# Kernel tuning notes

Measured on AMD Instinct MI355X. Metric: run time of the kernel, lower is better.

The kernel has to match this reference:

```python
import math
import jax, jax.numpy as jnp
import numpy as np

D_IN, R_S, T_MAX = 1024, 256, 2048
B, T = 8, 2048


def setup_inputs() -> dict:
    key = jax.random.key(0)
    ks = jax.random.split(key, 8)
    u = jax.random.normal(ks[0], (B, T, D_IN), dtype=jnp.float32)
    h0_r = jax.random.normal(ks[1], (B, R_S), dtype=jnp.float32)
    h0_i = jax.random.normal(ks[2], (B, R_S), dtype=jnp.float32)
    # parameters (lambda_raw randomized instead of zeros so sigmoid is nontrivial)
    lambda_raw = jax.random.normal(ks[3], (R_S,), dtype=jnp.float32)
    # omega init exactly as in the torch module
    log_min, log_max = math.log(1.0 / T_MAX), math.log(math.pi)
    n = np.arange(1, R_S + 1, dtype=np.float32)
    weyl_freqs = n * math.pi / R_S
    log_freqs = np.exp(np.linspace(log_min, log_max, R_S, dtype=np.float32))
    omega = jnp.asarray(0.5 * weyl_freqs + 0.5 * log_freqs, dtype=jnp.float32)
    W_proj = jax.random.normal(ks[4], (R_S, D_IN), dtype=jnp.float32) / math.sqrt(D_IN)
    W_res = jax.random.normal(ks[5], (2 * R_S, D_IN), dtype=jnp.float32) / math.sqrt(D_IN)
    ln_gamma = jnp.ones((2 * R_S,), dtype=jnp.float32)
    ln_beta = jnp.zeros((2 * R_S,), dtype=jnp.float32)
    return {"u": u, "h0_r": h0_r, "h0_i": h0_i, "lambda_raw": lambda_raw,
            "omega": omega, "W_proj": W_proj, "W_res": W_res,
            "ln_gamma": ln_gamma, "ln_beta": ln_beta}


def _layernorm(x, gamma, beta, eps=1e-5):
    mu = jnp.mean(x, axis=-1, keepdims=True)
    var = jnp.mean(jnp.square(x - mu), axis=-1, keepdims=True)
    return (x - mu) * jax.lax.rsqrt(var + eps) * gamma + beta


def reference(u, h0_r, h0_i, lambda_raw, omega, W_proj, W_res, ln_gamma, ln_beta):
    Bb, Tt, _ = u.shape
    lam = -jax.nn.sigmoid(lambda_raw) * 5.0                      # [R]
    t = jnp.arange(Tt, dtype=jnp.float32)                        # [T]
    decay = jnp.exp(lam[:, None] * t[None, :])                   # [R,T]
    phase = omega[:, None] * t[None, :]                          # [R,T]
    f_r = decay * jnp.cos(phase)
    f_i = decay * jnp.sin(phase)
    u_proj = jnp.einsum('btd,rd->brt', u, W_proj)                # [B,R,T]
    n_fft = 2 * Tt
    U_f = jnp.fft.rfft(u_proj, n=n_fft, axis=-1)                 # [B,R,F]
    F_r = jnp.fft.rfft(f_r, n=n_fft, axis=-1)[None]              # [1,R,F]
    F_i = jnp.fft.rfft(f_i, n=n_fft, axis=-1)[None]
    h_r = jnp.fft.irfft(U_f * F_r, n=n_fft, axis=-1)[..., :Tt]   # [B,R,T]
    h_i = jnp.fft.irfft(U_f * F_i, n=n_fft, axis=-1)[..., :Tt]
    # ZIR correction from initial state
    t_zir = t + 1.0
    decay_z = jnp.exp(lam[:, None] * t_zir[None, :])             # [R,T]
    phase_z = omega[:, None] * t_zir[None, :]
    f_r_z = decay_z * jnp.cos(phase_z)
    f_i_z = decay_z * jnp.sin(phase_z)
    h0r = h0_r[:, :, None]                                       # [B,R,1]
    h0i = h0_i[:, :, None]
    h_r = h_r + h0r * f_r_z[None] - h0i * f_i_z[None]
    h_i = h_i + h0r * f_i_z[None] + h0i * f_r_z[None]
    h_r = jnp.swapaxes(h_r, 1, 2)                                # [B,T,R]
    h_i = jnp.swapaxes(h_i, 1, 2)
    ssm_out = jnp.concatenate([h_r, h_i], axis=-1)               # [B,T,2R]
    res = jnp.einsum('btd,ed->bte', u, W_res)                    # [B,T,2R]
    out = _layernorm(ssm_out + res, ln_gamma, ln_beta)
    final_r = jax.lax.stop_gradient(h_r[:, -1])
    final_i = jax.lax.stop_gradient(h_i[:, -1])
    return out, final_r, final_i
```

## Files before the change

### kernel.cpp

```cpp
#include <hip/hip_runtime.h>
#include <math.h>

#define T_LEN 2048
#define BB    8
#define RS    256
#define DIN   1024
#define NE    768
#define M_TOT (BB * T_LEN)
#define LCH   32
#define NCH   (T_LEN / LCH)
#define OUT_MAIN (M_TOT * 512)

typedef unsigned short ushort;
typedef unsigned int   uint;
typedef short  short8  __attribute__((ext_vector_type(8)));
typedef float  f32x4   __attribute__((ext_vector_type(4)));
typedef ushort ushort8 __attribute__((ext_vector_type(8)));

__device__ __forceinline__ ushort f2bf_rn(float x) {
    uint u = __float_as_uint(x);
    return (ushort)((u + 0x7FFFu + ((u >> 16) & 1u)) >> 16);
}
__device__ __forceinline__ float bf2f(ushort b) {
    return __uint_as_float(((uint)b) << 16);
}

__device__ __forceinline__ void gload16(const ushort* g, ushort* l) {
    __builtin_amdgcn_global_load_lds(
        (const __attribute__((address_space(1))) uint*)g,
        (__attribute__((address_space(3))) uint*)l, 16, 0, 0);
}

#define N8U  (M_TOT * DIN / 8)
#define N8WP (RS * DIN / 8)
#define N8WR (2 * RS * DIN / 8)
#define N8TOT (N8U + N8WP + N8WR)

__global__ __launch_bounds__(256) void split_kernel(
    const float* __restrict__ u, const float* __restrict__ wp,
    const float* __restrict__ wr, ushort* __restrict__ Uhi,
    ushort* __restrict__ Ulo, ushort* __restrict__ Whi, ushort* __restrict__ Wlo)
{
    const int i = blockIdx.x * 256 + threadIdx.x;
    if (i >= N8TOT) return;
    const float* src; ushort* hi; ushort* lo; int j;
    if (i < N8U)              { src = u;  hi = Uhi; lo = Ulo; j = i; }
    else if (i < N8U + N8WP)  { src = wp; hi = Whi; lo = Wlo; j = i - N8U; }
    else                      { src = wr; hi = Whi + (size_t)RS * DIN;
                                lo = Wlo + (size_t)RS * DIN; j = i - N8U - N8WP; }
    const float4 x0 = ((const float4*)src)[(size_t)j * 2 + 0];
    const float4 x1 = ((const float4*)src)[(size_t)j * 2 + 1];
    const float xs[8] = {x0.x, x0.y, x0.z, x0.w, x1.x, x1.y, x1.z, x1.w};
    ushort8 hv, lv;
#pragma unroll
    for (int k = 0; k < 8; ++k) {
        const ushort hb = f2bf_rn(xs[k]);
        hv[k] = hb;
        lv[k] = f2bf_rn(xs[k] - bf2f(hb));
    }
    ((ushort8*)hi)[j] = hv;
    ((ushort8*)lo)[j] = lv;
}

#define Bb 128
#define BK 32

__global__ __launch_bounds__(256) void gemm_mfma(
    const ushort* __restrict__ Uh, const ushort* __restrict__ Ul,
    const ushort* __restrict__ Wh, const ushort* __restrict__ Wl,
    float* __restrict__ C)
{
    __shared__ ushort Ah[Bb * BK], Al[Bb * BK], Bh[Bb * BK], Bl[Bb * BK];
    const int tid  = threadIdx.x;
    const int bn   = blockIdx.x;
    const int bm   = blockIdx.y;
    const int wid  = tid >> 6;
    const int lane = tid & 63;
    const int wr   = wid >> 1, wc = wid & 1;
    const int fr   = lane & 15;
    const int fq   = lane >> 4;

    const int srow = tid >> 2;
    const int skk  = (tid & 3) * 8;
    const ushort* gAh = Uh + (size_t)(bm * 128 + srow) * DIN + skk;
    const ushort* gAl = Ul + (size_t)(bm * 128 + srow) * DIN + skk;
    const ushort* gBh = Wh + (size_t)(bn * 128 + srow) * DIN + skk;
    const ushort* gBl = Wl + (size_t)(bn * 128 + srow) * DIN + skk;
    ushort* lAh0 = Ah + tid * 8; ushort* lAh1 = Ah + 64 * BK + tid * 8;
    ushort* lAl0 = Al + tid * 8; ushort* lAl1 = Al + 64 * BK + tid * 8;
    ushort* lBh0 = Bh + tid * 8; ushort* lBh1 = Bh + 64 * BK + tid * 8;
    ushort* lBl0 = Bl + tid * 8; ushort* lBl1 = Bl + 64 * BK + tid * 8;
    const size_t rstep = (size_t)64 * DIN;

    f32x4 acc[4][4];
#pragma unroll
    for (int m = 0; m < 4; ++m)
#pragma unroll
        for (int n = 0; n < 4; ++n) acc[m][n] = (f32x4){0.f, 0.f, 0.f, 0.f};

    for (int kk = 0; kk < DIN; kk += BK) {
        gload16(gAh + kk, lAh0); gload16(gAh + kk + rstep, lAh1);
        gload16(gAl + kk, lAl0); gload16(gAl + kk + rstep, lAl1);
        gload16(gBh + kk, lBh0); gload16(gBh + kk + rstep, lBh1);
        gload16(gBl + kk, lBl0); gload16(gBl + kk + rstep, lBl1);
        __syncthreads();

        short8 ah[4], al[4], bh[4], bl[4];
#pragma unroll
        for (int m = 0; m < 4; ++m) {
            const int row = wr * 64 + m * 16 + fr;
            ah[m] = *(const short8*)&Ah[row * BK + fq * 8];
            al[m] = *(const short8*)&Al[row * BK + fq * 8];
        }
#pragma unroll
        for (int n = 0; n < 4; ++n) {
            const int col = wc * 64 + n * 16 + fr;
            bh[n] = *(const short8*)&Bh[col * BK + fq * 8];
            bl[n] = *(const short8*)&Bl[col * BK + fq * 8];
        }
#pragma unroll
        for (int m = 0; m < 4; ++m)
#pragma unroll
            for (int n = 0; n < 4; ++n) {
                acc[m][n] = __builtin_amdgcn_mfma_f32_16x16x32_bf16(ah[m], bh[n], acc[m][n], 0, 0, 0);
                acc[m][n] = __builtin_amdgcn_mfma_f32_16x16x32_bf16(ah[m], bl[n], acc[m][n], 0, 0, 0);
                acc[m][n] = __builtin_amdgcn_mfma_f32_16x16x32_bf16(al[m], bh[n], acc[m][n], 0, 0, 0);
            }
        __syncthreads();
    }

    const int crow0 = bm * 128 + wr * 64;
    const int ccol0 = bn * 128 + wc * 64;
#pragma unroll
    for (int m = 0; m < 4; ++m) {
        const int row = crow0 + m * 16 + fq * 4;
#pragma unroll
        for (int n = 0; n < 4; ++n) {
            const int col = ccol0 + n * 16 + fr;
#pragma unroll
            for (int j = 0; j < 4; ++j)
                C[(size_t)(row + j) * NE + col] = acc[m][n][j];
        }
    }
}

__device__ inline void pole(const float* __restrict__ lraw, const float* __restrict__ om,
                            int r, float& zr, float& zi, float& lam, float& o)
{
    const float x   = lraw[r];
    const float sig = 1.f / (1.f + expf(-x));
    lam = -5.f * sig;
    o   = om[r];
    const float er = expf(lam);
    zr = er * cosf(o);
    zi = er * sinf(o);
}

__global__ __launch_bounds__(256) void carry_kernel(
    const float* __restrict__ C, const float* __restrict__ lraw,
    const float* __restrict__ om, float2* __restrict__ carry)
{
    const int c = blockIdx.x, b = blockIdx.y, r = threadIdx.x;
    const int m0 = b * T_LEN + c * LCH;
    float zr, zi, lam, o;
    pole(lraw, om, r, zr, zi, lam, o);
    const float* p = C + (size_t)m0 * NE + r;
    float hr = 0.f, hi = 0.f;
#pragma unroll 8
    for (int s = 0; s < LCH; ++s) {
        const float u  = p[(size_t)s * NE];
        const float nr = zr * hr - zi * hi + u;
        const float ni = zr * hi + zi * hr;
        hr = nr; hi = ni;
    }
    carry[(size_t)(b * NCH + c) * RS + r] = make_float2(hr, hi);
}

__global__ __launch_bounds__(256) void chunk_scan_kernel(
    const float2* __restrict__ carry, const float* __restrict__ h0r,
    const float* __restrict__ h0i, const float* __restrict__ lraw,
    const float* __restrict__ om, float2* __restrict__ S, float* __restrict__ out)
{
    const int b = blockIdx.x, r = threadIdx.x;
    __shared__ float2 cs[32 * RS];
    float zr, zi, lam, o;
    pole(lraw, om, r, zr, zi, lam, o);
    const float eL  = expf(lam * (float)LCH);
    const float zLr = eL * cosf(o * (float)LCH);
    const float zLi = eL * sinf(o * (float)LCH);
    float sr = h0r[b * RS + r];
    float si = h0i[b * RS + r];
    for (int half = 0; half < 2; ++half) {
        __syncthreads();
        const float4* src = (const float4*)(carry + ((size_t)b * NCH + half * 32) * RS);
        float4* dst = (float4*)cs;
        for (int i = r; i < 32 * RS / 2; i += 256) dst[i] = src[i];
        __syncthreads();
        for (int cc = 0; cc < 32; ++cc) {
            const int c = half * 32 + cc;
            S[((size_t)b * NCH + c) * RS + r] = make_float2(sr, si);
            const float2 k = cs[cc * RS + r];
            const float nr = zLr * sr - zLi * si + k.x;
            const float ni = zLr * si + zLi * sr + k.y;
            sr = nr; si = ni;
        }
    }
    out[OUT_MAIN + b * RS + r]           = sr;
    out[OUT_MAIN + BB * RS + b * RS + r] = si;
}

__global__ __launch_bounds__(256) void scan_ln_kernel(
    const float* __restrict__ C, const float2* __restrict__ S,
    const float* __restrict__ lraw, const float* __restrict__ om,
    const float* __restrict__ gamma, const float* __restrict__ beta,
    float* __restrict__ out)
{
    const int c = blockIdx.x, b = blockIdx.y, r = threadIdx.x;
    __shared__ float tile[8][NE];
    const int m0 = b * T_LEN + c * LCH;
    float zr, zi, lam, o;
    pole(lraw, om, r, zr, zi, lam, o);
    float2 st = S[(size_t)(b * NCH + c) * RS + r];
    const int wid = r >> 6, lane = r & 63;
    const float4 g0  = *(const float4*)&gamma[lane * 8];
    const float4 g1  = *(const float4*)&gamma[lane * 8 + 4];
    const float4 be0 = *(const float4*)&beta[lane * 8];
    const float4 be1 = *(const float4*)&beta[lane * 8 + 4];

    float4 rv[6];
    {
        const float4* src = (const float4*)(C + (size_t)m0 * NE);
#pragma unroll
        for (int k = 0; k < 6; ++k) rv[k] = src[r + 256 * k];
#pragma unroll
        for (int k = 0; k < 6; ++k) ((float4*)tile)[r + 256 * k] = rv[k];
    }

    for (int batch = 0; batch < 4; ++batch) {
        __syncthreads();
        if (batch < 3) {
            const float4* src = (const float4*)(C + (size_t)(m0 + (batch + 1) * 8) * NE);
#pragma unroll
            for (int k = 0; k < 6; ++k) rv[k] = src[r + 256 * k];
        }
#pragma unroll
        for (int s = 0; s < 8; ++s) {
            const float u  = tile[s][r];
            const float hr = zr * st.x - zi * st.y + u;
            const float hi = zr * st.y + zi * st.x;
            st.x = hr; st.y = hi;
            tile[s][256 + r] = hr + tile[s][256 + r];
            tile[s][512 + r] = hi + tile[s][512 + r];
        }
        __syncthreads();
#pragma unroll
        for (int rr = 0; rr < 2; ++rr) {
            const int s = wid * 2 + rr;
            const int m = m0 + batch * 8 + s;
            const float4 x0 = *(const float4*)&tile[s][256 + lane * 8];
            const float4 x1 = *(const float4*)&tile[s][256 + lane * 8 + 4];
            float s1 = (x0.x + x0.y) + (x0.z + x0.w) + (x1.x + x1.y) + (x1.z + x1.w);
            float s2 = (x0.x * x0.x + x0.y * x0.y) + (x0.z * x0.z + x0.w * x0.w)
                     + (x1.x * x1.x + x1.y * x1.y) + (x1.z * x1.z + x1.w * x1.w);
#pragma unroll
            for (int off = 1; off < 64; off <<= 1) {
                s1 += __shfl_xor(s1, off);
                s2 += __shfl_xor(s2, off);
            }
            const float mu   = s1 * (1.f / 512.f);
            const float var  = s2 * (1.f / 512.f) - mu * mu;
            const float rstd = rsqrtf(var + 1e-5f);
            float4 o0, o1;
            o0.x = (x0.x - mu) * rstd * g0.x + be0.x;
            o0.y = (x0.y - mu) * rstd * g0.y + be0.y;
            o0.z = (x0.z - mu) * rstd * g0.z + be0.z;
            o0.w = (x0.w - mu) * rstd * g0.w + be0.w;
            o1.x = (x1.x - mu) * rstd * g1.x + be1.x;
            o1.y = (x1.y - mu) * rstd * g1.y + be1.y;
            o1.z = (x1.z - mu) * rstd * g1.z + be1.z;
            o1.w = (x1.w - mu) * rstd * g1.w + be1.w;
            *(float4*)&out[(size_t)m * 512 + lane * 8]     = o0;
            *(float4*)&out[(size_t)m * 512 + lane * 8 + 4] = o1;
        }
        __syncthreads();
        if (batch < 3) {
#pragma unroll
            for (int k = 0; k < 6; ++k) ((float4*)tile)[r + 256 * k] = rv[k];
        }
    }
}

extern "C" void kernel_launch(void* const* d_in, const int* in_sizes, int n_in,
                              void* d_out, int out_size, void* d_ws, size_t ws_size,
                              hipStream_t stream)
{
    const float* u    = (const float*)d_in[0];
    const float* h0r  = (const float*)d_in[1];
    const float* h0i  = (const float*)d_in[2];
    const float* lraw = (const float*)d_in[3];
    const float* omg  = (const float*)d_in[4];
    const float* Wp   = (const float*)d_in[5];
    const float* Wr   = (const float*)d_in[6];
    const float* gam  = (const float*)d_in[7];
    const float* bet  = (const float*)d_in[8];
    float* out = (float*)d_out;

    float*  C     = (float*)d_ws;
    float2* carry = (float2*)(C + (size_t)M_TOT * NE);
    float2* S     = carry + (size_t)BB * NCH * RS;
    ushort* Uhi   = (ushort*)(S + (size_t)BB * NCH * RS);
    ushort* Ulo   = Uhi + (size_t)M_TOT * DIN;
    ushort* Whi   = Ulo + (size_t)M_TOT * DIN;
    ushort* Wlo   = Whi + (size_t)NE * DIN;

    split_kernel<<<N8TOT / 256, 256, 0, stream>>>(u, Wp, Wr, Uhi, Ulo, Whi, Wlo);
    gemm_mfma<<<dim3(NE / 128, M_TOT / 128), 256, 0, stream>>>(Uhi, Ulo, Whi, Wlo, C);
    carry_kernel<<<dim3(NCH, BB), 256, 0, stream>>>(C, lraw, omg, carry);
    chunk_scan_kernel<<<BB, 256, 0, stream>>>(carry, h0r, h0i, lraw, omg, S, out);
    scan_ln_kernel<<<dim3(NCH, BB), 256, 0, stream>>>(C, (const float2*)S, lraw, omg, gam, bet, out);
}
```

Before: 258.6 us.

## Fold chunk-prefix scan into scan_ln kernel and remap GEMM block order for XCDs

Removes the serial single-block-per-batch chunk_scan kernel: each scan_ln block now recomputes its own starting state by scanning the preceding chunk carries and adding the h0 zero-input response directly. The LN kernel also drops the shared-memory staging of C and reads it straight from global memory, using a smaller LDS tile. The GEMM launch becomes 1D with a swizzled block id that groups the blocks handled by each of the 8 XCDs. The trade-off is redundant carry-scan work in later chunks (up to 63 steps) and loss of prefetch overlap in the LN pass.

```diff
diff --git a/kernel.cpp b/kernel.cpp
--- a/kernel.cpp
+++ b/kernel.cpp
@@ -72,8 +72,10 @@
 {
     __shared__ ushort Ah[Bb * BK], Al[Bb * BK], Bh[Bb * BK], Bl[Bb * BK];
     const int tid  = threadIdx.x;
-    const int bn   = blockIdx.x;
-    const int bm   = blockIdx.y;
+    const int id   = blockIdx.x;
+    const int sid  = (id & 7) * 96 + (id >> 3);
+    const int bn   = sid % 6;
+    const int bm   = sid / 6;
     const int wid  = tid >> 6;
     const int lane = tid & 63;
     const int wr   = wid >> 1, wc = wid & 1;
@@ -176,89 +178,65 @@
     carry[(size_t)(b * NCH + c) * RS + r] = make_float2(hr, hi);
 }
 
-__global__ __launch_bounds__(256) void chunk_scan_kernel(
-    const float2* __restrict__ carry, const float* __restrict__ h0r,
-    const float* __restrict__ h0i, const float* __restrict__ lraw,
-    const float* __restrict__ om, float2* __restrict__ S, float* __restrict__ out)
-{
-    const int b = blockIdx.x, r = threadIdx.x;
-    __shared__ float2 cs[32 * RS];
+__global__ __launch_bounds__(256) void scan_ln_kernel(
+    const float* __restrict__ C, const float2* __restrict__ carry,
+    const float* __restrict__ h0r, const float* __restrict__ h0i,
+    const float* __restrict__ lraw, const float* __restrict__ om,
+    const float* __restrict__ gamma, const float* __restrict__ beta,
+    float* __restrict__ out)
+{
+    const int c = blockIdx.x, b = blockIdx.y, r = threadIdx.x;
+    __shared__ float xt[8][512];
+    const int m0 = b * T_LEN + c * LCH;
     float zr, zi, lam, o;
     pole(lraw, om, r, zr, zi, lam, o);
+
     const float eL  = expf(lam * (float)LCH);
     const float zLr = eL * cosf(o * (float)LCH);
     const float zLi = eL * sinf(o * (float)LCH);
-    float sr = h0r[b * RS + r];
-    float si = h0i[b * RS + r];
-    for (int half = 0; half < 2; ++half) {
-        __syncthreads();
-        const float4* src = (const float4*)(carry + ((size_t)b * NCH + half * 32) * RS);
-        float4* dst = (float4*)cs;
-        for (int i = r; i < 32 * RS / 2; i += 256) dst[i] = src[i];
-        __syncthreads();
-        for (int cc = 0; cc < 32; ++cc) {
-            const int c = half * 32 + cc;
-            S[((size_t)b * NCH + c) * RS + r] = make_float2(sr, si);
-            const float2 k = cs[cc * RS + r];
-            const float nr = zLr * sr - zLi * si + k.x;
-            const float ni = zLr * si + zLi * sr + k.y;
-            sr = nr; si = ni;
-        }
-    }
-    out[OUT_MAIN + b * RS + r]           = sr;
-    out[OUT_MAIN + BB * RS + b * RS + r] = si;
-}
-
-__global__ __launch_bounds__(256) void scan_ln_kernel(
-    const float* __restrict__ C, const float2* __restrict__ S,
-    const float* __restrict__ lraw, const float* __restrict__ om,
-    const float* __restrict__ gamma, const float* __restrict__ beta,
-    float* __restrict__ out)
-{
-    const int c = blockIdx.x, b = blockIdx.y, r = threadIdx.x;
-    __shared__ float tile[8][NE];
-    const int m0 = b * T_LEN + c * LCH;
-    float zr, zi, lam, o;
-    pole(lraw, om, r, zr, zi, lam, o);
-    float2 st = S[(size_t)(b * NCH + c) * RS + r];
+    float ar = 0.f, ai = 0.f;
+    const float2* cp = carry + (size_t)b * NCH * RS + r;
+    for (int j = 0; j < c; ++j) {
+        const float2 k = cp[(size_t)j * RS];
+        const float nr = zLr * ar - zLi * ai + k.x;
+        const float ni = zLr * ai + zLi * ar + k.y;
+        ar = nr; ai = ni;
+    }
+    const float tL  = (float)(LCH * c);
+    const float dz  = expf(lam * tL);
+    const float pzr = dz * cosf(o * tL);
+    const float pzi = dz * sinf(o * tL);
+    const float h0R = h0r[b * RS + r];
+    const float h0I = h0i[b * RS + r];
+    float2 st;
+    st.x = ar + h0R * pzr - h0I * pzi;
+    st.y = ai + h0R * pzi + h0I * pzr;
+
     const int wid = r >> 6, lane = r & 63;
     const float4 g0  = *(const float4*)&gamma[lane * 8];
     const float4 g1  = *(const float4*)&gamma[lane * 8 + 4];
     const float4 be0 = *(const float4*)&beta[lane * 8];
     const float4 be1 = *(const float4*)&beta[lane * 8 + 4];
 
-    float4 rv[6];
-    {
-        const float4* src = (const float4*)(C + (size_t)m0 * NE);
-#pragma unroll
-        for (int k = 0; k < 6; ++k) rv[k] = src[r + 256 * k];
-#pragma unroll
-        for (int k = 0; k < 6; ++k) ((float4*)tile)[r + 256 * k] = rv[k];
-    }
-
     for (int batch = 0; batch < 4; ++batch) {
-        __syncthreads();
-        if (batch < 3) {
-            const float4* src = (const float4*)(C + (size_t)(m0 + (batch + 1) * 8) * NE);
-#pragma unroll
-            for (int k = 0; k < 6; ++k) rv[k] = src[r + 256 * k];
-        }
+        const int s0 = batch * 8;
 #pragma unroll
         for (int s = 0; s < 8; ++s) {
-            const float u  = tile[s][r];
+            const int m = m0 + s0 + s;
+            const float u  = C[(size_t)m * NE + r];
             const float hr = zr * st.x - zi * st.y + u;
             const float hi = zr * st.y + zi * st.x;
             st.x = hr; st.y = hi;
-            tile[s][256 + r] = hr + tile[s][256 + r];
-            tile[s][512 + r] = hi + tile[s][512 + r];
+            xt[s][r]       = hr + C[(size_t)m * NE + 256 + r];
+            xt[s][256 + r] = hi + C[(size_t)m * NE + 512 + r];
         }
         __syncthreads();
 #pragma unroll
         for (int rr = 0; rr < 2; ++rr) {
             const int s = wid * 2 + rr;
-            const int m = m0 + batch * 8 + s;
-            const float4 x0 = *(const float4*)&tile[s][256 + lane * 8];
-            const float4 x1 = *(const float4*)&tile[s][256 + lane * 8 + 4];
+            const int m = m0 + s0 + s;
+            const float4 x0 = *(const float4*)&xt[s][lane * 8];
+            const float4 x1 = *(const float4*)&xt[s][lane * 8 + 4];
             float s1 = (x0.x + x0.y) + (x0.z + x0.w) + (x1.x + x1.y) + (x1.z + x1.w);
             float s2 = (x0.x * x0.x + x0.y * x0.y) + (x0.z * x0.z + x0.w * x0.w)
                      + (x1.x * x1.x + x1.y * x1.y) + (x1.z * x1.z + x1.w * x1.w);
@@ -283,10 +261,11 @@
             *(float4*)&out[(size_t)m * 512 + lane * 8 + 4] = o1;
         }
         __syncthreads();
-        if (batch < 3) {
-#pragma unroll
-            for (int k = 0; k < 6; ++k) ((float4*)tile)[r + 256 * k] = rv[k];
-        }
+    }
+
+    if (c == NCH - 1) {
+        out[OUT_MAIN + b * RS + r]           = st.x;
+        out[OUT_MAIN + BB * RS + b * RS + r] = st.y;
     }
 }
 
@@ -307,15 +286,14 @@
 
     float*  C     = (float*)d_ws;
     float2* carry = (float2*)(C + (size_t)M_TOT * NE);
-    float2* S     = carry + (size_t)BB * NCH * RS;
-    ushort* Uhi   = (ushort*)(S + (size_t)BB * NCH * RS);
+    ushort* Uhi   = (ushort*)(carry + (size_t)BB * NCH * RS);
     ushort* Ulo   = Uhi + (size_t)M_TOT * DIN;
     ushort* Whi   = Ulo + (size_t)M_TOT * DIN;
     ushort* Wlo   = Whi + (size_t)NE * DIN;
 
     split_kernel<<<N8TOT / 256, 256, 0, stream>>>(u, Wp, Wr, Uhi, Ulo, Whi, Wlo);
-    gemm_mfma<<<dim3(NE / 128, M_TOT / 128), 256, 0, stream>>>(Uhi, Ulo, Whi, Wlo, C);
+    gemm_mfma<<<768, 256, 0, stream>>>(Uhi, Ulo, Whi, Wlo, C);
     carry_kernel<<<dim3(NCH, BB), 256, 0, stream>>>(C, lraw, omg, carry);
-    chunk_scan_kernel<<<BB, 256, 0, stream>>>(carry, h0r, h0i, lraw, omg, S, out);
-    scan_ln_kernel<<<dim3(NCH, BB), 256, 0, stream>>>(C, (const float2*)S, lraw, omg, gam, bet, out);
-}
+    scan_ln_kernel<<<dim3(NCH, BB), 256, 0, stream>>>(C, (const float2*)carry,
+                                                      h0r, h0i, lraw, omg, gam, bet, out);
+}
```

Measured after the change: 227.0 us. -12.2%, faster.

## Fuse activation bf16 hi/lo split into GEMM with register prefetch and block swizzle

Applied to the files above, without the earlier changes.

Removes the separate pass that split u into bf16 hi/lo arrays. The GEMM now loads fp32 u directly, prefetching the next K tile into registers, and converts it in-kernel to hi/lo by truncation before storing to LDS. Blocks use a swizzled 1D grid order so that groups of blocks share A and B tiles in cache. The scan/LN kernel drops its LDS staging of C and reads C straight from global memory. This cuts a large amount of global traffic (the bf16 copies of u) in exchange for extra VALU work and register pressure inside the GEMM. Truncation instead of round-to-nearest for the hi part slightly changes numerics.

```diff
diff --git a/kernel.cpp b/kernel.cpp
--- a/kernel.cpp
+++ b/kernel.cpp
@@ -31,23 +31,20 @@
         (__attribute__((address_space(3))) uint*)l, 16, 0, 0);
 }
 
-#define N8U  (M_TOT * DIN / 8)
 #define N8WP (RS * DIN / 8)
 #define N8WR (2 * RS * DIN / 8)
-#define N8TOT (N8U + N8WP + N8WR)
-
-__global__ __launch_bounds__(256) void split_kernel(
-    const float* __restrict__ u, const float* __restrict__ wp,
-    const float* __restrict__ wr, ushort* __restrict__ Uhi,
-    ushort* __restrict__ Ulo, ushort* __restrict__ Whi, ushort* __restrict__ Wlo)
+#define N8W  (N8WP + N8WR)
+
+__global__ __launch_bounds__(256) void splitW_kernel(
+    const float* __restrict__ wp, const float* __restrict__ wr,
+    ushort* __restrict__ Whi, ushort* __restrict__ Wlo)
 {
     const int i = blockIdx.x * 256 + threadIdx.x;
-    if (i >= N8TOT) return;
+    if (i >= N8W) return;
     const float* src; ushort* hi; ushort* lo; int j;
-    if (i < N8U)              { src = u;  hi = Uhi; lo = Ulo; j = i; }
-    else if (i < N8U + N8WP)  { src = wp; hi = Whi; lo = Wlo; j = i - N8U; }
-    else                      { src = wr; hi = Whi + (size_t)RS * DIN;
-                                lo = Wlo + (size_t)RS * DIN; j = i - N8U - N8WP; }
+    if (i < N8WP) { src = wp; hi = Whi; lo = Wlo; j = i; }
+    else          { src = wr; hi = Whi + (size_t)RS * DIN;
+                    lo = Wlo + (size_t)RS * DIN; j = i - N8WP; }
     const float4 x0 = ((const float4*)src)[(size_t)j * 2 + 0];
     const float4 x1 = ((const float4*)src)[(size_t)j * 2 + 1];
     const float xs[8] = {x0.x, x0.y, x0.z, x0.w, x1.x, x1.y, x1.z, x1.w};
@@ -64,16 +61,31 @@
 
 #define Bb 128
 #define BK 32
+#define KTILES (DIN / BK)
+
+__device__ __forceinline__ void cvt_split8(const float4 a, const float4 b,
+                                           ushort8& hv, ushort8& lv)
+{
+    const float xs[8] = {a.x, a.y, a.z, a.w, b.x, b.y, b.z, b.w};
+#pragma unroll
+    for (int j = 0; j < 8; ++j) {
+        const uint u = __float_as_uint(xs[j]);
+        hv[j] = (ushort)(u >> 16);
+        const float lo = xs[j] - __uint_as_float(u & 0xFFFF0000u);
+        lv[j] = (ushort)(__float_as_uint(lo) >> 16);
+    }
+}
 
 __global__ __launch_bounds__(256) void gemm_mfma(
-    const ushort* __restrict__ Uh, const ushort* __restrict__ Ul,
-    const ushort* __restrict__ Wh, const ushort* __restrict__ Wl,
-    float* __restrict__ C)
+    const float* __restrict__ U, const ushort* __restrict__ Wh,
+    const ushort* __restrict__ Wl, float* __restrict__ C)
 {
     __shared__ ushort Ah[Bb * BK], Al[Bb * BK], Bh[Bb * BK], Bl[Bb * BK];
     const int tid  = threadIdx.x;
-    const int bn   = blockIdx.x;
-    const int bm   = blockIdx.y;
+    const int id   = blockIdx.x;
+    const int sid  = (id & 7) * 96 + (id >> 3);
+    const int bn   = sid % 6;
+    const int bm   = sid / 6;
     const int wid  = tid >> 6;
     const int lane = tid & 63;
     const int wr   = wid >> 1, wc = wid & 1;
@@ -82,52 +94,92 @@
 
     const int srow = tid >> 2;
     const int skk  = (tid & 3) * 8;
-    const ushort* gAh = Uh + (size_t)(bm * 128 + srow) * DIN + skk;
-    const ushort* gAl = Ul + (size_t)(bm * 128 + srow) * DIN + skk;
     const ushort* gBh = Wh + (size_t)(bn * 128 + srow) * DIN + skk;
     const ushort* gBl = Wl + (size_t)(bn * 128 + srow) * DIN + skk;
-    ushort* lAh0 = Ah + tid * 8; ushort* lAh1 = Ah + 64 * BK + tid * 8;
-    ushort* lAl0 = Al + tid * 8; ushort* lAl1 = Al + 64 * BK + tid * 8;
     ushort* lBh0 = Bh + tid * 8; ushort* lBh1 = Bh + 64 * BK + tid * 8;
     ushort* lBl0 = Bl + tid * 8; ushort* lBl1 = Bl + 64 * BK + tid * 8;
     const size_t rstep = (size_t)64 * DIN;
 
+    const float* gA = U + (size_t)(bm * 128 + (tid >> 2)) * DIN + (tid & 3) * 8;
+    ushort* aDstH0 = Ah + tid * 8; ushort* aDstH1 = Ah + 2048 + tid * 8;
+    ushort* aDstL0 = Al + tid * 8; ushort* aDstL1 = Al + 2048 + tid * 8;
+
     f32x4 acc[4][4];
 #pragma unroll
     for (int m = 0; m < 4; ++m)
 #pragma unroll
         for (int n = 0; n < 4; ++n) acc[m][n] = (f32x4){0.f, 0.f, 0.f, 0.f};
 
-    for (int kk = 0; kk < DIN; kk += BK) {
-        gload16(gAh + kk, lAh0); gload16(gAh + kk + rstep, lAh1);
-        gload16(gAl + kk, lAl0); gload16(gAl + kk + rstep, lAl1);
-        gload16(gBh + kk, lBh0); gload16(gBh + kk + rstep, lBh1);
-        gload16(gBl + kk, lBl0); gload16(gBl + kk + rstep, lBl1);
-        __syncthreads();
-
-        short8 ah[4], al[4], bh[4], bl[4];
-#pragma unroll
-        for (int m = 0; m < 4; ++m) {
-            const int row = wr * 64 + m * 16 + fr;
-            ah[m] = *(const short8*)&Ah[row * BK + fq * 8];
-            al[m] = *(const short8*)&Al[row * BK + fq * 8];
-        }
-#pragma unroll
-        for (int n = 0; n < 4; ++n) {
-            const int col = wc * 64 + n * 16 + fr;
-            bh[n] = *(const short8*)&Bh[col * BK + fq * 8];
-            bl[n] = *(const short8*)&Bl[col * BK + fq * 8];
-        }
-#pragma unroll
-        for (int m = 0; m < 4; ++m)
-#pragma unroll
-            for (int n = 0; n < 4; ++n) {
-                acc[m][n] = __builtin_amdgcn_mfma_f32_16x16x32_bf16(ah[m], bh[n], acc[m][n], 0, 0, 0);
-                acc[m][n] = __builtin_amdgcn_mfma_f32_16x16x32_bf16(ah[m], bl[n], acc[m][n], 0, 0, 0);
-                acc[m][n] = __builtin_amdgcn_mfma_f32_16x16x32_bf16(al[m], bh[n], acc[m][n], 0, 0, 0);
-            }
-        __syncthreads();
-    }
+#define LOAD_A(dst, kt)                                                        \
+    do {                                                                       \
+        dst[0] = *(const float4*)(gA + (kt) * BK);                             \
+        dst[1] = *(const float4*)(gA + (kt) * BK + 4);                         \
+        dst[2] = *(const float4*)(gA + rstep + (kt) * BK);                     \
+        dst[3] = *(const float4*)(gA + rstep + (kt) * BK + 4);                 \
+    } while (0)
+
+#define STAGE_A(rg)                                                            \
+    do {                                                                       \
+        ushort8 hv, lv;                                                        \
+        cvt_split8(rg[0], rg[1], hv, lv);                                      \
+        *(ushort8*)aDstH0 = hv; *(ushort8*)aDstL0 = lv;                        \
+        cvt_split8(rg[2], rg[3], hv, lv);                                      \
+        *(ushort8*)aDstH1 = hv; *(ushort8*)aDstL1 = lv;                        \
+    } while (0)
+
+#define COMPUTE_STEP                                                           \
+    do {                                                                       \
+        short8 ah[4], al[4], bh[4], bl[4];                                     \
+        _Pragma("unroll")                                                      \
+        for (int m = 0; m < 4; ++m) {                                          \
+            const int row = wr * 64 + m * 16 + fr;                             \
+            ah[m] = *(const short8*)&Ah[row * BK + fq * 8];                    \
+            al[m] = *(const short8*)&Al[row * BK + fq * 8];                    \
+        }                                                                      \
+        _Pragma("unroll")                                                      \
+        for (int n = 0; n < 4; ++n) {                                          \
+            const int col = wc * 64 + n * 16 + fr;                             \
+            bh[n] = *(const short8*)&Bh[col * BK + fq * 8];                    \
+            bl[n] = *(const short8*)&Bl[col * BK + fq * 8];                    \
+        }                                                                      \
+        _Pragma("unroll")                                                      \
+        for (int m = 0; m < 4; ++m)                                            \
+            _Pragma("unroll")                                                  \
+            for (int n = 0; n < 4; ++n) {                                      \
+                acc[m][n] = __builtin_amdgcn_mfma_f32_16x16x32_bf16(ah[m], bh[n], acc[m][n], 0, 0, 0); \
+                acc[m][n] = __builtin_amdgcn_mfma_f32_16x16x32_bf16(ah[m], bl[n], acc[m][n], 0, 0, 0); \
+                acc[m][n] = __builtin_amdgcn_mfma_f32_16x16x32_bf16(al[m], bh[n], acc[m][n], 0, 0, 0); \
+            }                                                                  \
+    } while (0)
+
+    float4 rA[4], rB_[4];
+    LOAD_A(rA, 0);
+
+    for (int kt = 0; kt < KTILES; kt += 2) {
+        {
+            const int kk = kt * BK;
+            gload16(gBh + kk, lBh0); gload16(gBh + kk + rstep, lBh1);
+            gload16(gBl + kk, lBl0); gload16(gBl + kk + rstep, lBl1);
+            STAGE_A(rA);
+            __syncthreads();
+            LOAD_A(rB_, kt + 1);
+            COMPUTE_STEP;
+            __syncthreads();
+        }
+        {
+            const int kk = (kt + 1) * BK;
+            gload16(gBh + kk, lBh0); gload16(gBh + kk + rstep, lBh1);
+            gload16(gBl + kk, lBl0); gload16(gBl + kk + rstep, lBl1);
+            STAGE_A(rB_);
+            __syncthreads();
+            if (kt + 2 < KTILES) LOAD_A(rA, kt + 2);
+            COMPUTE_STEP;
+            __syncthreads();
+        }
+    }
+#undef LOAD_A
+#undef STAGE_A
+#undef COMPUTE_STEP
 
     const int crow0 = bm * 128 + wr * 64;
     const int ccol0 = bn * 128 + wc * 64;
@@ -216,7 +268,7 @@
     float* __restrict__ out)
 {
     const int c = blockIdx.x, b = blockIdx.y, r = threadIdx.x;
-    __shared__ float tile[8][NE];
+    __shared__ float xt[8][512];
     const int m0 = b * T_LEN + c * LCH;
     float zr, zi, lam, o;
     pole(lraw, om, r, zr, zi, lam, o);
@@ -227,38 +279,25 @@
     const float4 be0 = *(const float4*)&beta[lane * 8];
     const float4 be1 = *(const float4*)&beta[lane * 8 + 4];
 
-    float4 rv[6];
-    {
-        const float4* src = (const float4*)(C + (size_t)m0 * NE);
-#pragma unroll
-        for (int k = 0; k < 6; ++k) rv[k] = src[r + 256 * k];
-#pragma unroll
-        for (int k = 0; k < 6; ++k) ((float4*)tile)[r + 256 * k] = rv[k];
-    }
-
     for (int batch = 0; batch < 4; ++batch) {
-        __syncthreads();
-        if (batch < 3) {
-            const float4* src = (const float4*)(C + (size_t)(m0 + (batch + 1) * 8) * NE);
-#pragma unroll
-            for (int k = 0; k < 6; ++k) rv[k] = src[r + 256 * k];
-        }
+        const int s0 = batch * 8;
 #pragma unroll
         for (int s = 0; s < 8; ++s) {
-            const float u  = tile[s][r];
+            const int m = m0 + s0 + s;
+            const float u  = C[(size_t)m * NE + r];
             const float hr = zr * st.x - zi * st.y + u;
             const float hi = zr * st.y + zi * st.x;
             st.x = hr; st.y = hi;
-            tile[s][256 + r] = hr + tile[s][256 + r];
-            tile[s][512 + r] = hi + tile[s][512 + r];
+            xt[s][r]       = hr + C[(size_t)m * NE + 256 + r];
+            xt[s][256 + r] = hi + C[(size_t)m * NE + 512 + r];
         }
         __syncthreads();
 #pragma unroll
         for (int rr = 0; rr < 2; ++rr) {
             const int s = wid * 2 + rr;
-            const int m = m0 + batch * 8 + s;
-            const float4 x0 = *(const float4*)&tile[s][256 + lane * 8];
-            const float4 x1 = *(const float4*)&tile[s][256 + lane * 8 + 4];
+            const int m = m0 + s0 + s;
+            const float4 x0 = *(const float4*)&xt[s][lane * 8];
+            const float4 x1 = *(const float4*)&xt[s][lane * 8 + 4];
             float s1 = (x0.x + x0.y) + (x0.z + x0.w) + (x1.x + x1.y) + (x1.z + x1.w);
             float s2 = (x0.x * x0.x + x0.y * x0.y) + (x0.z * x0.z + x0.w * x0.w)
                      + (x1.x * x1.x + x1.y * x1.y) + (x1.z * x1.z + x1.w * x1.w);
@@ -283,10 +322,6 @@
             *(float4*)&out[(size_t)m * 512 + lane * 8 + 4] = o1;
         }
         __syncthreads();
-        if (batch < 3) {
-#pragma unroll
-            for (int k = 0; k < 6; ++k) ((float4*)tile)[r + 256 * k] = rv[k];
-        }
     }
 }
 
@@ -308,13 +343,11 @@
     float*  C     = (float*)d_ws;
     float2* carry = (float2*)(C + (size_t)M_TOT * NE);
     float2* S     = carry + (size_t)BB * NCH * RS;
-    ushort* Uhi   = (ushort*)(S + (size_t)BB * NCH * RS);
-    ushort* Ulo   = Uhi + (size_t)M_TOT * DIN;
-    ushort* Whi   = Ulo + (size_t)M_TOT * DIN;
+    ushort* Whi   = (ushort*)(S + (size_t)BB * NCH * RS);
     ushort* Wlo   = Whi + (size_t)NE * DIN;
 
-    split_kernel<<<N8TOT / 256, 256, 0, stream>>>(u, Wp, Wr, Uhi, Ulo, Whi, Wlo);
-    gemm_mfma<<<dim3(NE / 128, M_TOT / 128), 256, 0, stream>>>(Uhi, Ulo, Whi, Wlo, C);
+    splitW_kernel<<<N8W / 256, 256, 0, stream>>>(Wp, Wr, Whi, Wlo);
+    gemm_mfma<<<768, 256, 0, stream>>>(u, Whi, Wlo, C);
     carry_kernel<<<dim3(NCH, BB), 256, 0, stream>>>(C, lraw, omg, carry);
     chunk_scan_kernel<<<BB, 256, 0, stream>>>(carry, h0r, h0i, lraw, omg, S, out);
     scan_ln_kernel<<<dim3(NCH, BB), 256, 0, stream>>>(C, (const float2*)S, lraw, omg, gam, bet, out);
```

Result: no change. 257.4 us (-0.5%).

## Halve scan chunk length, swizzle GEMM block order, stream C directly in scan-LN

Applied to the files above, without the earlier changes.

Chunk length drops from 32 to 16, which doubles the number of chunks. That gives the carry and scan-LN kernels twice as many blocks to spread across the GPU. The serial chunk scan now walks 128 chunks per batch in four shared-memory batches instead of two. The GEMM moves to a 1D grid with an XCD-aware swizzle (id&7)*96+(id>>3), so blocks that share tiles run on the same L2. The scan-LN kernel drops the register-prefetched shared tile of C, reads C straight from global memory and stages only the 512 LayerNorm inputs in LDS. This gives up the explicit prefetch overlap but lowers LDS use.

```diff
diff --git a/kernel.cpp b/kernel.cpp
--- a/kernel.cpp
+++ b/kernel.cpp
@@ -7,7 +7,7 @@
 #define DIN   1024
 #define NE    768
 #define M_TOT (BB * T_LEN)
-#define LCH   32
+#define LCH   16
 #define NCH   (T_LEN / LCH)
 #define OUT_MAIN (M_TOT * 512)
 
@@ -72,8 +72,10 @@
 {
     __shared__ ushort Ah[Bb * BK], Al[Bb * BK], Bh[Bb * BK], Bl[Bb * BK];
     const int tid  = threadIdx.x;
-    const int bn   = blockIdx.x;
-    const int bm   = blockIdx.y;
+    const int id   = blockIdx.x;
+    const int sid  = (id & 7) * 96 + (id >> 3);
+    const int bn   = sid % 6;
+    const int bm   = sid / 6;
     const int wid  = tid >> 6;
     const int lane = tid & 63;
     const int wr   = wid >> 1, wc = wid & 1;
@@ -190,14 +192,14 @@
     const float zLi = eL * sinf(o * (float)LCH);
     float sr = h0r[b * RS + r];
     float si = h0i[b * RS + r];
-    for (int half = 0; half < 2; ++half) {
-        __syncthreads();
-        const float4* src = (const float4*)(carry + ((size_t)b * NCH + half * 32) * RS);
+    for (int q = 0; q < 4; ++q) {
+        __syncthreads();
+        const float4* src = (const float4*)(carry + ((size_t)b * NCH + q * 32) * RS);
         float4* dst = (float4*)cs;
         for (int i = r; i < 32 * RS / 2; i += 256) dst[i] = src[i];
         __syncthreads();
         for (int cc = 0; cc < 32; ++cc) {
-            const int c = half * 32 + cc;
+            const int c = q * 32 + cc;
             S[((size_t)b * NCH + c) * RS + r] = make_float2(sr, si);
             const float2 k = cs[cc * RS + r];
             const float nr = zLr * sr - zLi * si + k.x;
@@ -216,7 +218,7 @@
     float* __restrict__ out)
 {
     const int c = blockIdx.x, b = blockIdx.y, r = threadIdx.x;
-    __shared__ float tile[8][NE];
+    __shared__ float xt[8][512];
     const int m0 = b * T_LEN + c * LCH;
     float zr, zi, lam, o;
     pole(lraw, om, r, zr, zi, lam, o);
@@ -227,38 +229,25 @@
     const float4 be0 = *(const float4*)&beta[lane * 8];
     const float4 be1 = *(const float4*)&beta[lane * 8 + 4];
 
-    float4 rv[6];
-    {
-        const float4* src = (const float4*)(C + (size_t)m0 * NE);
-#pragma unroll
-        for (int k = 0; k < 6; ++k) rv[k] = src[r + 256 * k];
-#pragma unroll
-        for (int k = 0; k < 6; ++k) ((float4*)tile)[r + 256 * k] = rv[k];
-    }
-
-    for (int batch = 0; batch < 4; ++batch) {
-        __syncthreads();
-        if (batch < 3) {
-            const float4* src = (const float4*)(C + (size_t)(m0 + (batch + 1) * 8) * NE);
-#pragma unroll
-            for (int k = 0; k < 6; ++k) rv[k] = src[r + 256 * k];
-        }
+    for (int batch = 0; batch < LCH / 8; ++batch) {
+        const int s0 = batch * 8;
 #pragma unroll
         for (int s = 0; s < 8; ++s) {
-            const float u  = tile[s][r];
+            const int m = m0 + s0 + s;
+            const float u  = C[(size_t)m * NE + r];
             const float hr = zr * st.x - zi * st.y + u;
             const float hi = zr * st.y + zi * st.x;
             st.x = hr; st.y = hi;
-            tile[s][256 + r] = hr + tile[s][256 + r];
-            tile[s][512 + r] = hi + tile[s][512 + r];
+            xt[s][r]       = hr + C[(size_t)m * NE + 256 + r];
+            xt[s][256 + r] = hi + C[(size_t)m * NE + 512 + r];
         }
         __syncthreads();
 #pragma unroll
         for (int rr = 0; rr < 2; ++rr) {
             const int s = wid * 2 + rr;
-            const int m = m0 + batch * 8 + s;
-            const float4 x0 = *(const float4*)&tile[s][256 + lane * 8];
-            const float4 x1 = *(const float4*)&tile[s][256 + lane * 8 + 4];
+            const int m = m0 + s0 + s;
+            const float4 x0 = *(const float4*)&xt[s][lane * 8];
+            const float4 x1 = *(const float4*)&xt[s][lane * 8 + 4];
             float s1 = (x0.x + x0.y) + (x0.z + x0.w) + (x1.x + x1.y) + (x1.z + x1.w);
             float s2 = (x0.x * x0.x + x0.y * x0.y) + (x0.z * x0.z + x0.w * x0.w)
                      + (x1.x * x1.x + x1.y * x1.y) + (x1.z * x1.z + x1.w * x1.w);
@@ -283,10 +272,6 @@
             *(float4*)&out[(size_t)m * 512 + lane * 8 + 4] = o1;
         }
         __syncthreads();
-        if (batch < 3) {
-#pragma unroll
-            for (int k = 0; k < 6; ++k) ((float4*)tile)[r + 256 * k] = rv[k];
-        }
     }
 }
 
@@ -314,7 +299,7 @@
     ushort* Wlo   = Whi + (size_t)NE * DIN;
 
     split_kernel<<<N8TOT / 256, 256, 0, stream>>>(u, Wp, Wr, Uhi, Ulo, Whi, Wlo);
-    gemm_mfma<<<dim3(NE / 128, M_TOT / 128), 256, 0, stream>>>(Uhi, Ulo, Whi, Wlo, C);
+    gemm_mfma<<<768, 256, 0, stream>>>(Uhi, Ulo, Whi, Wlo, C);
     carry_kernel<<<dim3(NCH, BB), 256, 0, stream>>>(C, lraw, omg, carry);
     chunk_scan_kernel<<<BB, 256, 0, stream>>>(carry, h0r, h0i, lraw, omg, S, out);
     scan_ln_kernel<<<dim3(NCH, BB), 256, 0, stream>>>(C, (const float2*)S, lraw, omg, gam, bet, out);
```

New measurement: 240.2 us. -7.1%, faster.
